# Performance work log

Measured on AMD Instinct MI355X. Metric: run time of the kernel, lower is better.

## Reference

```python
import jax, jax.numpy as jnp
import numpy as np

N_HEAD = 8

def _l2norm(x, eps=1e-12):
    # F.normalize(p=2, dim=-1): x / max(||x||_2, eps)
    return x / jnp.maximum(jnp.linalg.norm(x, axis=-1, keepdims=True), eps)

def setup_inputs() -> dict:
    key = jax.random.key(0)
    ks = jax.random.split(key, 9)
    B, L, E = 2, 2048, 512
    s = 0.02
    return {
        "query": jax.random.normal(ks[0], (B, L, E), dtype=jnp.float32),
        "Wq": s * jax.random.normal(ks[1], (E, E), dtype=jnp.float32),
        "bq": jnp.zeros((E,), dtype=jnp.float32),
        "Wk": s * jax.random.normal(ks[2], (E, E), dtype=jnp.float32),
        "bk": jnp.zeros((E,), dtype=jnp.float32),
        "Wv": s * jax.random.normal(ks[3], (E, E), dtype=jnp.float32),
        "bv": jnp.zeros((E,), dtype=jnp.float32),
        "Wo": s * jax.random.normal(ks[4], (E, E), dtype=jnp.float32),
        "bo": jnp.zeros((E,), dtype=jnp.float32),
    }

def reference(query, Wq, bq, Wk, bk, Wv, bv, Wo, bo):
    B, L, E = query.shape
    H = N_HEAD
    hd = E // H
    # Faithful to torch: .view(tgt_len, bsz, E) is a RESHAPE, not a transpose.
    x = query.reshape(L, B, E)
    q = jax.nn.relu(x @ Wq.T + bq)
    k = jax.nn.relu(x @ Wk.T + bk)
    v = x @ Wv.T + bv
    q = _l2norm(q)
    k = _l2norm(k)
    # (L, B, E) -> (L, B*H, hd) -> (B*H, L, hd)
    q_ = q.reshape(L, B * H, hd).transpose(1, 0, 2)
    k_ = k.reshape(L, B * H, hd).transpose(1, 0, 2)
    v_ = v.reshape(L, B * H, hd).transpose(1, 0, 2)
    # Causal linear attention: cumulative outer-product of k,v then contract with q.
    kv = jnp.einsum('nld,nlm->nldm', k_, v_)      # [B*H, L, hd, hd]
    kv_cum = jnp.cumsum(kv, axis=1)
    out = jnp.einsum('nld,nldm->nlm', q_, kv_cum)  # [B*H, L, hd]
    out = out.transpose(1, 0, 2).reshape(L, B, E)
    out = out @ Wo.T + bo
    return out.reshape(B, L, E)
```

## Files before the change

### kernel.cpp

```cpp
#include <hip/hip_runtime.h>
#include <hip/hip_bf16.h>

typedef __attribute__((ext_vector_type(8))) short short8;
typedef __attribute__((ext_vector_type(4))) float f32x4;
using bf16 = __hip_bfloat16;

__device__ __forceinline__ unsigned short f2bf(float f) {
    unsigned u = __float_as_uint(f);
    u += 0x7fff + ((u >> 16) & 1);
    return (unsigned short)(u >> 16);
}
__device__ __forceinline__ float bf2f(unsigned short s) {
    return __uint_as_float(((unsigned)s) << 16);
}
__device__ __forceinline__ void gl_lds16(const unsigned short* g, unsigned short* l) {
    __builtin_amdgcn_global_load_lds(
        (const __attribute__((address_space(1))) unsigned int*)g,
        (__attribute__((address_space(3))) unsigned int*)l, 16, 0, 0);
}


__global__ __launch_bounds__(256) void pack_kernel(
    const float* __restrict__ X, const float* __restrict__ Wq, const float* __restrict__ Wk,
    const float* __restrict__ Wv, const float* __restrict__ Wo,
    bf16* __restrict__ Xp, bf16* __restrict__ Wqp, bf16* __restrict__ Wkp,
    bf16* __restrict__ Wvp, bf16* __restrict__ Wop, float* __restrict__ ssq)
{
    __shared__ __align__(16) unsigned short sm[4096];
    int id = blockIdx.x;
    int tid = threadIdx.x;
    if (id < 8) {
        int zi = id * 1024 + tid * 4;
        *(float4*)&ssq[zi] = make_float4(0.f, 0.f, 0.f, 0.f);
    }
    const float* src; unsigned short* dst; int g, sc;
    if (id < 512) { src = X; dst = (unsigned short*)Xp; g = id >> 3; sc = id & 7; }
    else {
        int t = id - 512; int wsel = t >> 6; int u = t & 63;
        g = u >> 3; sc = u & 7;
        src = (wsel == 0) ? Wq : ((wsel == 1) ? Wk : ((wsel == 2) ? Wv : Wo));
        dst = (unsigned short*)((wsel == 0) ? Wqp : ((wsel == 1) ? Wkp : ((wsel == 2) ? Wvp : Wop)));
    }
    int r = tid >> 2, kq = tid & 3;
    const float* sp = src + (size_t)(g * 64 + r) * 512 + sc * 64 + kq * 16;
    #pragma unroll
    for (int i = 0; i < 4; ++i) {
        float4 v = *(const float4*)(sp + i * 4);
        int kk = kq * 16 + i * 4;
        int sl = kk >> 3, el = kk & 7;
        ushort4 u4;
        u4.x = f2bf(v.x); u4.y = f2bf(v.y); u4.z = f2bf(v.z); u4.w = f2bf(v.w);
        *(ushort4*)&sm[(sl * 64 + r) * 8 + el] = u4;
    }
    __syncthreads();
    unsigned short* dp = dst + (size_t)g * 32768 + sc * 4096;
    *(uint4*)(dp + tid * 16)     = *(const uint4*)&sm[tid * 16];
    *(uint4*)(dp + tid * 16 + 8) = *(const uint4*)&sm[tid * 16 + 8];
}

__global__ __launch_bounds__(256) void qkv_gemm_kernel(
    const bf16* __restrict__ Xp,
    const bf16* __restrict__ W0p, const bf16* __restrict__ W1p, const bf16* __restrict__ W2p,
    const float* __restrict__ b0, const float* __restrict__ b1, const float* __restrict__ b2,
    bf16* __restrict__ O0, bf16* __restrict__ O1, bf16* __restrict__ O2,
    float* __restrict__ ssq)
{
    __shared__ __align__(16) unsigned short smem[8192];
    unsigned short* As = smem;
    unsigned short* Bs = smem + 2048;
    int z = blockIdx.z;
    const unsigned short* Wg = (const unsigned short*)((z == 0) ? W0p : ((z == 1) ? W1p : W2p));
    const float* bias = (z == 0) ? b0 : ((z == 1) ? b1 : b2);
    unsigned short* Out = (unsigned short*)((z == 0) ? O0 : ((z == 1) ? O1 : O2));
    const unsigned short* Ag = (const unsigned short*)Xp;

    int g  = blockIdx.x;
    int gB = blockIdx.y * 2;
    int m0 = g * 64;
    int n0 = blockIdx.y * 128;
    int tid = threadIdx.x;
    int lane = tid & 63;
    int w = tid >> 6;
    int wm = (w >> 1) * 32;
    int wn = (w & 1) * 64;
    int fr = lane & 15, qf = lane >> 4;

    f32x4 zero4 = {0.f, 0.f, 0.f, 0.f};
    f32x4 acc[2][4];
    #pragma unroll
    for (int t = 0; t < 2; ++t)
        #pragma unroll
        for (int u = 0; u < 4; ++u) acc[t][u] = zero4;

    for (int kw = 0; kw < 16; ++kw) {
        int s0 = kw * 4;
        __syncthreads();
        gl_lds16(Ag + ((size_t)(g * 64 + s0 + w) * 64 + lane) * 8, As + w * 512);
        gl_lds16(Wg + ((size_t)(gB * 64 + s0 + w) * 64 + lane) * 8, Bs + w * 1024);
        gl_lds16(Wg + ((size_t)((gB + 1) * 64 + s0 + w) * 64 + lane) * 8, Bs + w * 1024 + 512);
        __syncthreads();
        short8 af[2], bfr[4];
        #pragma unroll
        for (int t = 0; t < 2; ++t) af[t] = *(const short8*)&As[(qf * 64 + wm + t * 16 + fr) * 8];
        #pragma unroll
        for (int u = 0; u < 4; ++u) bfr[u] = *(const short8*)&Bs[(qf * 128 + wn + u * 16 + fr) * 8];
        #pragma unroll
        for (int t = 0; t < 2; ++t)
            #pragma unroll
            for (int u = 0; u < 4; ++u)
                acc[t][u] = __builtin_amdgcn_mfma_f32_16x16x32_bf16(af[t], bfr[u], acc[t][u], 0, 0, 0);
    }

    bool relu = (z < 2);
    int rb = qf * 4;
    #pragma unroll
    for (int t = 0; t < 2; ++t)
        #pragma unroll
        for (int u = 0; u < 4; ++u) {
            float bv = bias[n0 + wn + u * 16 + fr];
            #pragma unroll
            for (int r = 0; r < 4; ++r) {
                float v = acc[t][u][r] + bv;
                if (relu) v = fmaxf(v, 0.f);
                acc[t][u][r] = v;
            }
        }
    if (relu) {
        #pragma unroll
        for (int t = 0; t < 2; ++t)
            #pragma unroll
            for (int r = 0; r < 4; ++r) {
                float s = 0.f;
                #pragma unroll
                for (int u = 0; u < 4; ++u) s += acc[t][u][r] * acc[t][u][r];
                #pragma unroll
                for (int off = 1; off < 16; off <<= 1) s += __shfl_xor(s, off, 64);
                if (fr == 0) atomicAdd(&ssq[z * 4096 + m0 + wm + t * 16 + rb + r], s);
            }
    }
    __syncthreads();
    #pragma unroll
    for (int t = 0; t < 2; ++t)
        #pragma unroll
        for (int u = 0; u < 4; ++u)
            #pragma unroll
            for (int r = 0; r < 4; ++r)
                smem[(wm + t * 16 + rb + r) * 128 + wn + u * 16 + fr] = f2bf(acc[t][u][r]);
    __syncthreads();
    #pragma unroll
    for (int rep = 0; rep < 4; ++rep) {
        int idx8 = rep * 256 + tid;
        int row = idx8 >> 4, col8 = (idx8 & 15) * 8;
        *(uint4*)(Out + (size_t)(m0 + row) * 512 + n0 + col8) = *(const uint4*)&smem[row * 128 + col8];
    }
}

__global__ __launch_bounds__(256) void chunk_kv_kernel(
    const bf16* __restrict__ Kb, const bf16* __restrict__ Vb,
    const float* __restrict__ ssq, float* __restrict__ ScT, bf16* __restrict__ Vt_g)
{
    int n = blockIdx.x >> 4, c = blockIdx.x & 15;
    int b = n >> 3, h = n & 7;
    __shared__ float Ks[64 * 64];
    __shared__ float Vs[64 * 64];
    const unsigned short* Kg = (const unsigned short*)Kb;
    const unsigned short* Vg = (const unsigned short*)Vb;
    int tid = threadIdx.x;
    int td = tid >> 4, tm = tid & 15;
    int d0 = td * 4, m0 = tm * 4;
    int vm = tid & 63, vj0 = (tid >> 6) * 16;
    float acc[4][4] = {};
    for (int half = 0; half < 2; ++half) {
        __syncthreads();
        #pragma unroll
        for (int rep = 0; rep < 4; ++rep) {
            int idx = rep * 1024 + tid * 4;
            int j = idx >> 6, d = idx & 63;
            int grow = (c * 128 + half * 64 + j) * 2 + b;
            ushort4 ku = *(const ushort4*)&Kg[(size_t)grow * 512 + h * 64 + d];
            ushort4 vu = *(const ushort4*)&Vg[(size_t)grow * 512 + h * 64 + d];
            float rk = 1.f / fmaxf(sqrtf(ssq[4096 + grow]), 1e-12f);
            *(float4*)&Ks[j * 64 + d] = make_float4(bf2f(ku.x), bf2f(ku.y), bf2f(ku.z), bf2f(ku.w));
            *(float4*)&Vs[j * 64 + d] = make_float4(bf2f(vu.x) * rk, bf2f(vu.y) * rk,
                                                    bf2f(vu.z) * rk, bf2f(vu.w) * rk);
        }
        __syncthreads();
        for (int j = 0; j < 64; ++j) {
            float4 kv = *(const float4*)&Ks[j * 64 + d0];
            float4 vv = *(const float4*)&Vs[j * 64 + m0];
            acc[0][0] += kv.x*vv.x; acc[0][1] += kv.x*vv.y; acc[0][2] += kv.x*vv.z; acc[0][3] += kv.x*vv.w;
            acc[1][0] += kv.y*vv.x; acc[1][1] += kv.y*vv.y; acc[1][2] += kv.y*vv.z; acc[1][3] += kv.y*vv.w;
            acc[2][0] += kv.z*vv.x; acc[2][1] += kv.z*vv.y; acc[2][2] += kv.z*vv.z; acc[2][3] += kv.z*vv.w;
            acc[3][0] += kv.w*vv.x; acc[3][1] += kv.w*vv.y; acc[3][2] += kv.w*vv.z; acc[3][3] += kv.w*vv.w;
        }
        unsigned short tmp[16];
        #pragma unroll
        for (int i = 0; i < 16; ++i) tmp[i] = f2bf(Vs[(vj0 + i) * 64 + vm]);
        size_t vtoff = (size_t)n * 131072 + (size_t)vm * 2048 + c * 128 + half * 64 + vj0;
        *(uint4*)((unsigned short*)Vt_g + vtoff)     = *(uint4*)&tmp[0];
        *(uint4*)((unsigned short*)Vt_g + vtoff + 8) = *(uint4*)&tmp[8];
    }
    float* outp = ScT + (size_t)blockIdx.x * 4096;
    #pragma unroll
    for (int j2 = 0; j2 < 4; ++j2) {
        float4 o4 = make_float4(acc[0][j2], acc[1][j2], acc[2][j2], acc[3][j2]);
        *(float4*)&outp[(m0 + j2) * 64 + d0] = o4;
    }
}

__global__ __launch_bounds__(256) void prefix_kernel(const float* __restrict__ ScT, bf16* __restrict__ SpT)
{
    int n = blockIdx.x >> 4;
    int idx = ((blockIdx.x & 15) << 8) + threadIdx.x;
    size_t base = (size_t)n * 65536 + idx;
    unsigned short* sp = (unsigned short*)SpT;
    float run = 0.f;
    #pragma unroll
    for (int c = 0; c < 16; ++c) {
        size_t off = base + (size_t)c * 4096;
        sp[off] = f2bf(run);
        run += ScT[off];
    }
}

__global__ __launch_bounds__(256) void attn_kernel(
    const bf16* __restrict__ Qb, const bf16* __restrict__ Kb,
    const bf16* __restrict__ Vt_g, const bf16* __restrict__ SpT_g,
    const float* __restrict__ ssq, bf16* __restrict__ AOb)
{
    int n = blockIdx.x >> 4, c = blockIdx.x & 15;
    int b = n >> 3, h = n & 7;
    __shared__ unsigned short Qs[128 * 72];
    __shared__ unsigned short Ks[128 * 72];
    __shared__ unsigned short Vt[64 * 136];
    __shared__ unsigned short Ps[4 * 32 * 40];
    int tid = threadIdx.x;
    int lane = tid & 63;
    int w = tid >> 6;
    int fr = lane & 15, q = lane >> 4;

    const unsigned short* Qg = (const unsigned short*)Qb;
    const unsigned short* Kg = (const unsigned short*)Kb;
    const unsigned short* Vg = (const unsigned short*)Vt_g;

    #pragma unroll
    for (int rep = 0; rep < 4; ++rep) {
        int idx = rep * 256 + tid;
        int l = idx >> 3, dc = (idx & 7) * 8;
        size_t goff = (size_t)((c * 128 + l) * 2 + b) * 512 + h * 64 + dc;
        *(uint4*)&Qs[l * 72 + dc] = *(const uint4*)(Qg + goff);
        *(uint4*)&Ks[l * 72 + dc] = *(const uint4*)(Kg + goff);
    }
    #pragma unroll
    for (int rep = 0; rep < 4; ++rep) {
        int idx = rep * 256 + tid;
        int m = idx >> 4, jc = (idx & 15) * 8;
        *(uint4*)&Vt[m * 136 + jc] =
            *(const uint4*)(Vg + (size_t)n * 131072 + (size_t)m * 2048 + c * 128 + jc);
    }
    __syncthreads();

    short8 qf[2][2];
    #pragma unroll
    for (int lt = 0; lt < 2; ++lt)
        #pragma unroll
        for (int kh = 0; kh < 2; ++kh)
            qf[lt][kh] = *(const short8*)&Qs[(w * 32 + lt * 16 + fr) * 72 + kh * 32 + q * 8];

    f32x4 zero4 = {0.f, 0.f, 0.f, 0.f};
    f32x4 oacc[2][4];
    #pragma unroll
    for (int lt = 0; lt < 2; ++lt)
        #pragma unroll
        for (int mt = 0; mt < 4; ++mt) oacc[lt][mt] = zero4;

    const unsigned short* spg = (const unsigned short*)SpT_g + (size_t)blockIdx.x * 4096;
    #pragma unroll
    for (int mt = 0; mt < 4; ++mt) {
        #pragma unroll
        for (int kh = 0; kh < 2; ++kh) {
            short8 sf = *(const short8*)&spg[(mt * 16 + fr) * 64 + kh * 32 + q * 8];
            oacc[0][mt] = __builtin_amdgcn_mfma_f32_16x16x32_bf16(qf[0][kh], sf, oacc[0][mt], 0, 0, 0);
            oacc[1][mt] = __builtin_amdgcn_mfma_f32_16x16x32_bf16(qf[1][kh], sf, oacc[1][mt], 0, 0, 0);
        }
    }

    unsigned short* myPs = &Ps[w * 1280];
    int rbase = q * 4;
    for (int jt = 0; jt <= w; ++jt) {
        f32x4 pacc[2][2];
        pacc[0][0] = zero4; pacc[0][1] = zero4; pacc[1][0] = zero4; pacc[1][1] = zero4;
        #pragma unroll
        for (int jt16 = 0; jt16 < 2; ++jt16) {
            #pragma unroll
            for (int kh = 0; kh < 2; ++kh) {
                short8 kf = *(const short8*)&Ks[(jt * 32 + jt16 * 16 + fr) * 72 + kh * 32 + q * 8];
                pacc[0][jt16] = __builtin_amdgcn_mfma_f32_16x16x32_bf16(qf[0][kh], kf, pacc[0][jt16], 0, 0, 0);
                pacc[1][jt16] = __builtin_amdgcn_mfma_f32_16x16x32_bf16(qf[1][kh], kf, pacc[1][jt16], 0, 0, 0);
            }
        }
        bool diag = (jt == w);
        #pragma unroll
        for (int lt = 0; lt < 2; ++lt)
            #pragma unroll
            for (int jt16 = 0; jt16 < 2; ++jt16)
                #pragma unroll
                for (int r = 0; r < 4; ++r) {
                    int ll = lt * 16 + rbase + r;
                    int jl = jt16 * 16 + fr;
                    float pv = pacc[lt][jt16][r];
                    if (diag && jl > ll) pv = 0.f;
                    myPs[ll * 40 + jl] = f2bf(pv);
                }
        short8 pf0 = *(const short8*)&myPs[fr * 40 + q * 8];
        short8 pf1 = *(const short8*)&myPs[(16 + fr) * 40 + q * 8];
        #pragma unroll
        for (int mt = 0; mt < 4; ++mt) {
            short8 vf = *(const short8*)&Vt[(mt * 16 + fr) * 136 + jt * 32 + q * 8];
            oacc[0][mt] = __builtin_amdgcn_mfma_f32_16x16x32_bf16(pf0, vf, oacc[0][mt], 0, 0, 0);
            oacc[1][mt] = __builtin_amdgcn_mfma_f32_16x16x32_bf16(pf1, vf, oacc[1][mt], 0, 0, 0);
        }
    }

    float rqv[2][4];
    #pragma unroll
    for (int lt = 0; lt < 2; ++lt)
        #pragma unroll
        for (int r = 0; r < 4; ++r) {
            int flat = (c * 128 + w * 32 + lt * 16 + rbase + r) * 2 + b;
            rqv[lt][r] = 1.f / fmaxf(sqrtf(ssq[flat]), 1e-12f);
        }
    __syncthreads();
    #pragma unroll
    for (int lt = 0; lt < 2; ++lt)
        #pragma unroll
        for (int mt = 0; mt < 4; ++mt)
            #pragma unroll
            for (int r = 0; r < 4; ++r)
                Qs[(w * 32 + lt * 16 + rbase + r) * 64 + mt * 16 + fr] = f2bf(oacc[lt][mt][r] * rqv[lt][r]);
    __syncthreads();
    #pragma unroll
    for (int rep = 0; rep < 4; ++rep) {
        int idx8 = rep * 256 + tid;
        int l = idx8 >> 3, m8 = (idx8 & 7) * 8;
        *(uint4*)((unsigned short*)AOb + (size_t)((c * 128 + l) * 2 + b) * 512 + h * 64 + m8) =
            *(const uint4*)&Qs[l * 64 + m8];
    }
}

__global__ __launch_bounds__(256) void oproj_kernel(
    const bf16* __restrict__ A, const bf16* __restrict__ Wop,
    const float* __restrict__ bias, float* __restrict__ Out)
{
    __shared__ __align__(16) unsigned short smem[16384];
    unsigned short* As = smem;
    unsigned short* Bs = smem + 2560;
    const unsigned short* Ag = (const unsigned short*)A;
    const unsigned short* Wg = (const unsigned short*)Wop;
    int m0 = blockIdx.x * 64;
    int gB = blockIdx.y * 2;
    int n0 = blockIdx.y * 128;
    int tid = threadIdx.x;
    int lane = tid & 63;
    int w = tid >> 6;
    int fr = lane & 15, qf = lane >> 4;
    int wm = (w >> 1) * 32;
    int wn = (w & 1) * 64;
    int srow = tid >> 2;
    int skk  = (tid & 3) * 8;

    f32x4 zero4 = {0.f, 0.f, 0.f, 0.f};
    f32x4 acc[2][4];
    #pragma unroll
    for (int t = 0; t < 2; ++t)
        #pragma unroll
        for (int u = 0; u < 4; ++u) acc[t][u] = zero4;

    for (int kw = 0; kw < 16; ++kw) {
        int k0 = kw * 32, s0 = kw * 4;
        __syncthreads();
        *(uint4*)&As[srow * 40 + skk] = *(const uint4*)(Ag + (size_t)(m0 + srow) * 512 + k0 + skk);
        gl_lds16(Wg + ((size_t)(gB * 64 + s0 + w) * 64 + lane) * 8, Bs + w * 1024);
        gl_lds16(Wg + ((size_t)((gB + 1) * 64 + s0 + w) * 64 + lane) * 8, Bs + w * 1024 + 512);
        __syncthreads();
        short8 af[2], bfr[4];
        #pragma unroll
        for (int t = 0; t < 2; ++t) af[t] = *(const short8*)&As[(wm + t * 16 + fr) * 40 + qf * 8];
        #pragma unroll
        for (int u = 0; u < 4; ++u) bfr[u] = *(const short8*)&Bs[(qf * 128 + wn + u * 16 + fr) * 8];
        #pragma unroll
        for (int t = 0; t < 2; ++t)
            #pragma unroll
            for (int u = 0; u < 4; ++u)
                acc[t][u] = __builtin_amdgcn_mfma_f32_16x16x32_bf16(af[t], bfr[u], acc[t][u], 0, 0, 0);
    }

    int rb = qf * 4;
    float* Cf = (float*)smem;
    __syncthreads();
    #pragma unroll
    for (int t = 0; t < 2; ++t)
        #pragma unroll
        for (int u = 0; u < 4; ++u) {
            float bv = bias[n0 + wn + u * 16 + fr];
            #pragma unroll
            for (int r = 0; r < 4; ++r)
                Cf[(wm + t * 16 + rb + r) * 128 + wn + u * 16 + fr] = acc[t][u][r] + bv;
        }
    __syncthreads();
    #pragma unroll
    for (int rep = 0; rep < 8; ++rep) {
        int idx = rep * 256 + tid;
        int row = idx >> 5, c4 = (idx & 31) * 4;
        *(float4*)(Out + (size_t)(m0 + row) * 512 + n0 + c4) = *(const float4*)&Cf[row * 128 + c4];
    }
}

extern "C" void kernel_launch(void* const* d_in, const int* in_sizes, int n_in,
                              void* d_out, int out_size, void* d_ws, size_t ws_size,
                              hipStream_t stream)
{
    (void)in_sizes; (void)n_in; (void)out_size; (void)ws_size;
    const float* x  = (const float*)d_in[0];
    const float* Wq = (const float*)d_in[1];
    const float* bq = (const float*)d_in[2];
    const float* Wk = (const float*)d_in[3];
    const float* bk = (const float*)d_in[4];
    const float* Wv = (const float*)d_in[5];
    const float* bv = (const float*)d_in[6];
    const float* Wo = (const float*)d_in[7];
    const float* bo = (const float*)d_in[8];
    float* out = (float*)d_out;

    float* ssq = (float*)d_ws;
    bf16* Xp  = (bf16*)(ssq + 8192);
    bf16* Wqp = Xp + 2097152;
    bf16* Wkp = Wqp + 262144;
    bf16* Wvp = Wkp + 262144;
    bf16* Wop = Wvp + 262144;
    bf16* Qb  = Wop + 262144;
    bf16* Kb  = Qb + 2097152;
    bf16* Vb  = Kb + 2097152;
    bf16* Vt  = Vb + 2097152;
    bf16* AOb = Vt + 2097152;
    bf16* SpT = AOb + 2097152;
    float* ScT = (float*)(SpT + 1048576);

    pack_kernel<<<768, 256, 0, stream>>>(x, Wq, Wk, Wv, Wo, Xp, Wqp, Wkp, Wvp, Wop, ssq);
    qkv_gemm_kernel<<<dim3(64, 4, 3), 256, 0, stream>>>(Xp, Wqp, Wkp, Wvp, bq, bk, bv, Qb, Kb, Vb, ssq);
    chunk_kv_kernel<<<dim3(256), 256, 0, stream>>>(Kb, Vb, ssq, ScT, Vt);
    prefix_kernel<<<dim3(256), 256, 0, stream>>>(ScT, SpT);
    attn_kernel<<<dim3(256), 256, 0, stream>>>(Qb, Kb, Vt, SpT, ssq, AOb);
    oproj_kernel<<<dim3(64, 4), 256, 0, stream>>>(AOb, Wop, bo, out);
}
```

Before: 123.6 us.

## Fuse all six stages into one cooperative persistent kernel with grid syncs

Replaces the six separate kernel launches (pack, QKV GEMM, chunk KV, prefix, attention, output projection) with one cooperative kernel of 256 blocks that runs each stage in turn, separated by grid-wide barriers. The aim is to remove per-launch overhead and the idle gaps between dependent kernels. In exchange each stage is limited to 256 blocks: the pack and QKV stages now loop over several work items per block, which lowers parallelism there. The single kernel also uses a larger shared-memory footprint, which may reduce occupancy.

After: 315.1 us. 155% more time.

```diff
diff --git a/kernel.cpp b/kernel.cpp
--- a/kernel.cpp
+++ b/kernel.cpp
@@ -1,5 +1,8 @@
 #include <hip/hip_runtime.h>
 #include <hip/hip_bf16.h>
+#include <hip/hip_cooperative_groups.h>
+
+namespace cg = cooperative_groups;
 
 typedef __attribute__((ext_vector_type(8))) short short8;
 typedef __attribute__((ext_vector_type(4))) float f32x4;
@@ -20,399 +23,385 @@
 }
 
 
-__global__ __launch_bounds__(256) void pack_kernel(
-    const float* __restrict__ X, const float* __restrict__ Wq, const float* __restrict__ Wk,
-    const float* __restrict__ Wv, const float* __restrict__ Wo,
+__global__ __launch_bounds__(256) void fused_kernel(
+    const float* __restrict__ X,
+    const float* __restrict__ Wq, const float* __restrict__ bq,
+    const float* __restrict__ Wk, const float* __restrict__ bk,
+    const float* __restrict__ Wv, const float* __restrict__ bv,
+    const float* __restrict__ Wo, const float* __restrict__ bo,
+    float* __restrict__ out,
     bf16* __restrict__ Xp, bf16* __restrict__ Wqp, bf16* __restrict__ Wkp,
-    bf16* __restrict__ Wvp, bf16* __restrict__ Wop, float* __restrict__ ssq)
+    bf16* __restrict__ Wvp, bf16* __restrict__ Wop,
+    bf16* __restrict__ Qb, bf16* __restrict__ Kb, bf16* __restrict__ Vb,
+    bf16* __restrict__ Vt_g, bf16* __restrict__ AOb, bf16* __restrict__ SpT,
+    float* __restrict__ ScT, float* __restrict__ ssq)
 {
-    __shared__ __align__(16) unsigned short sm[4096];
-    int id = blockIdx.x;
-    int tid = threadIdx.x;
-    if (id < 8) {
-        int zi = id * 1024 + tid * 4;
-        *(float4*)&ssq[zi] = make_float4(0.f, 0.f, 0.f, 0.f);
-    }
-    const float* src; unsigned short* dst; int g, sc;
-    if (id < 512) { src = X; dst = (unsigned short*)Xp; g = id >> 3; sc = id & 7; }
-    else {
-        int t = id - 512; int wsel = t >> 6; int u = t & 63;
-        g = u >> 3; sc = u & 7;
-        src = (wsel == 0) ? Wq : ((wsel == 1) ? Wk : ((wsel == 2) ? Wv : Wo));
-        dst = (unsigned short*)((wsel == 0) ? Wqp : ((wsel == 1) ? Wkp : ((wsel == 2) ? Wvp : Wop)));
-    }
-    int r = tid >> 2, kq = tid & 3;
-    const float* sp = src + (size_t)(g * 64 + r) * 512 + sc * 64 + kq * 16;
-    #pragma unroll
-    for (int i = 0; i < 4; ++i) {
-        float4 v = *(const float4*)(sp + i * 4);
-        int kk = kq * 16 + i * 4;
-        int sl = kk >> 3, el = kk & 7;
-        ushort4 u4;
-        u4.x = f2bf(v.x); u4.y = f2bf(v.y); u4.z = f2bf(v.z); u4.w = f2bf(v.w);
-        *(ushort4*)&sm[(sl * 64 + r) * 8 + el] = u4;
-    }
-    __syncthreads();
-    unsigned short* dp = dst + (size_t)g * 32768 + sc * 4096;
-    *(uint4*)(dp + tid * 16)     = *(const uint4*)&sm[tid * 16];
-    *(uint4*)(dp + tid * 16 + 8) = *(const uint4*)&sm[tid * 16 + 8];
-}
-
-__global__ __launch_bounds__(256) void qkv_gemm_kernel(
-    const bf16* __restrict__ Xp,
-    const bf16* __restrict__ W0p, const bf16* __restrict__ W1p, const bf16* __restrict__ W2p,
-    const float* __restrict__ b0, const float* __restrict__ b1, const float* __restrict__ b2,
-    bf16* __restrict__ O0, bf16* __restrict__ O1, bf16* __restrict__ O2,
-    float* __restrict__ ssq)
-{
-    __shared__ __align__(16) unsigned short smem[8192];
-    unsigned short* As = smem;
-    unsigned short* Bs = smem + 2048;
-    int z = blockIdx.z;
-    const unsigned short* Wg = (const unsigned short*)((z == 0) ? W0p : ((z == 1) ? W1p : W2p));
-    const float* bias = (z == 0) ? b0 : ((z == 1) ? b1 : b2);
-    unsigned short* Out = (unsigned short*)((z == 0) ? O0 : ((z == 1) ? O1 : O2));
-    const unsigned short* Ag = (const unsigned short*)Xp;
-
-    int g  = blockIdx.x;
-    int gB = blockIdx.y * 2;
-    int m0 = g * 64;
-    int n0 = blockIdx.y * 128;
-    int tid = threadIdx.x;
-    int lane = tid & 63;
-    int w = tid >> 6;
-    int wm = (w >> 1) * 32;
-    int wn = (w & 1) * 64;
-    int fr = lane & 15, qf = lane >> 4;
-
-    f32x4 zero4 = {0.f, 0.f, 0.f, 0.f};
-    f32x4 acc[2][4];
-    #pragma unroll
-    for (int t = 0; t < 2; ++t)
-        #pragma unroll
-        for (int u = 0; u < 4; ++u) acc[t][u] = zero4;
-
-    for (int kw = 0; kw < 16; ++kw) {
-        int s0 = kw * 4;
-        __syncthreads();
-        gl_lds16(Ag + ((size_t)(g * 64 + s0 + w) * 64 + lane) * 8, As + w * 512);
-        gl_lds16(Wg + ((size_t)(gB * 64 + s0 + w) * 64 + lane) * 8, Bs + w * 1024);
-        gl_lds16(Wg + ((size_t)((gB + 1) * 64 + s0 + w) * 64 + lane) * 8, Bs + w * 1024 + 512);
-        __syncthreads();
-        short8 af[2], bfr[4];
-        #pragma unroll
-        for (int t = 0; t < 2; ++t) af[t] = *(const short8*)&As[(qf * 64 + wm + t * 16 + fr) * 8];
-        #pragma unroll
-        for (int u = 0; u < 4; ++u) bfr[u] = *(const short8*)&Bs[(qf * 128 + wn + u * 16 + fr) * 8];
-        #pragma unroll
-        for (int t = 0; t < 2; ++t)
-            #pragma unroll
-            for (int u = 0; u < 4; ++u)
-                acc[t][u] = __builtin_amdgcn_mfma_f32_16x16x32_bf16(af[t], bfr[u], acc[t][u], 0, 0, 0);
-    }
-
-    bool relu = (z < 2);
-    int rb = qf * 4;
-    #pragma unroll
-    for (int t = 0; t < 2; ++t)
-        #pragma unroll
-        for (int u = 0; u < 4; ++u) {
-            float bv = bias[n0 + wn + u * 16 + fr];
-            #pragma unroll
-            for (int r = 0; r < 4; ++r) {
-                float v = acc[t][u][r] + bv;
-                if (relu) v = fmaxf(v, 0.f);
-                acc[t][u][r] = v;
-            }
-        }
-    if (relu) {
-        #pragma unroll
-        for (int t = 0; t < 2; ++t)
-            #pragma unroll
-            for (int r = 0; r < 4; ++r) {
-                float s = 0.f;
-                #pragma unroll
-                for (int u = 0; u < 4; ++u) s += acc[t][u][r] * acc[t][u][r];
-                #pragma unroll
-                for (int off = 1; off < 16; off <<= 1) s += __shfl_xor(s, off, 64);
-                if (fr == 0) atomicAdd(&ssq[z * 4096 + m0 + wm + t * 16 + rb + r], s);
-            }
-    }
-    __syncthreads();
-    #pragma unroll
-    for (int t = 0; t < 2; ++t)
-        #pragma unroll
-        for (int u = 0; u < 4; ++u)
-            #pragma unroll
-            for (int r = 0; r < 4; ++r)
-                smem[(wm + t * 16 + rb + r) * 128 + wn + u * 16 + fr] = f2bf(acc[t][u][r]);
-    __syncthreads();
-    #pragma unroll
-    for (int rep = 0; rep < 4; ++rep) {
-        int idx8 = rep * 256 + tid;
-        int row = idx8 >> 4, col8 = (idx8 & 15) * 8;
-        *(uint4*)(Out + (size_t)(m0 + row) * 512 + n0 + col8) = *(const uint4*)&smem[row * 128 + col8];
-    }
-}
-
-__global__ __launch_bounds__(256) void chunk_kv_kernel(
-    const bf16* __restrict__ Kb, const bf16* __restrict__ Vb,
-    const float* __restrict__ ssq, float* __restrict__ ScT, bf16* __restrict__ Vt_g)
-{
-    int n = blockIdx.x >> 4, c = blockIdx.x & 15;
-    int b = n >> 3, h = n & 7;
-    __shared__ float Ks[64 * 64];
-    __shared__ float Vs[64 * 64];
-    const unsigned short* Kg = (const unsigned short*)Kb;
-    const unsigned short* Vg = (const unsigned short*)Vb;
-    int tid = threadIdx.x;
-    int td = tid >> 4, tm = tid & 15;
-    int d0 = td * 4, m0 = tm * 4;
-    int vm = tid & 63, vj0 = (tid >> 6) * 16;
-    float acc[4][4] = {};
-    for (int half = 0; half < 2; ++half) {
-        __syncthreads();
-        #pragma unroll
-        for (int rep = 0; rep < 4; ++rep) {
-            int idx = rep * 1024 + tid * 4;
-            int j = idx >> 6, d = idx & 63;
-            int grow = (c * 128 + half * 64 + j) * 2 + b;
-            ushort4 ku = *(const ushort4*)&Kg[(size_t)grow * 512 + h * 64 + d];
-            ushort4 vu = *(const ushort4*)&Vg[(size_t)grow * 512 + h * 64 + d];
-            float rk = 1.f / fmaxf(sqrtf(ssq[4096 + grow]), 1e-12f);
-            *(float4*)&Ks[j * 64 + d] = make_float4(bf2f(ku.x), bf2f(ku.y), bf2f(ku.z), bf2f(ku.w));
-            *(float4*)&Vs[j * 64 + d] = make_float4(bf2f(vu.x) * rk, bf2f(vu.y) * rk,
-                                                    bf2f(vu.z) * rk, bf2f(vu.w) * rk);
-        }
-        __syncthreads();
-        for (int j = 0; j < 64; ++j) {
-            float4 kv = *(const float4*)&Ks[j * 64 + d0];
-            float4 vv = *(const float4*)&Vs[j * 64 + m0];
-            acc[0][0] += kv.x*vv.x; acc[0][1] += kv.x*vv.y; acc[0][2] += kv.x*vv.z; acc[0][3] += kv.x*vv.w;
-            acc[1][0] += kv.y*vv.x; acc[1][1] += kv.y*vv.y; acc[1][2] += kv.y*vv.z; acc[1][3] += kv.y*vv.w;
-            acc[2][0] += kv.z*vv.x; acc[2][1] += kv.z*vv.y; acc[2][2] += kv.z*vv.z; acc[2][3] += kv.z*vv.w;
-            acc[3][0] += kv.w*vv.x; acc[3][1] += kv.w*vv.y; acc[3][2] += kv.w*vv.z; acc[3][3] += kv.w*vv.w;
-        }
-        unsigned short tmp[16];
-        #pragma unroll
-        for (int i = 0; i < 16; ++i) tmp[i] = f2bf(Vs[(vj0 + i) * 64 + vm]);
-        size_t vtoff = (size_t)n * 131072 + (size_t)vm * 2048 + c * 128 + half * 64 + vj0;
-        *(uint4*)((unsigned short*)Vt_g + vtoff)     = *(uint4*)&tmp[0];
-        *(uint4*)((unsigned short*)Vt_g + vtoff + 8) = *(uint4*)&tmp[8];
-    }
-    float* outp = ScT + (size_t)blockIdx.x * 4096;
-    #pragma unroll
-    for (int j2 = 0; j2 < 4; ++j2) {
-        float4 o4 = make_float4(acc[0][j2], acc[1][j2], acc[2][j2], acc[3][j2]);
-        *(float4*)&outp[(m0 + j2) * 64 + d0] = o4;
-    }
-}
-
-__global__ __launch_bounds__(256) void prefix_kernel(const float* __restrict__ ScT, bf16* __restrict__ SpT)
-{
-    int n = blockIdx.x >> 4;
-    int idx = ((blockIdx.x & 15) << 8) + threadIdx.x;
-    size_t base = (size_t)n * 65536 + idx;
-    unsigned short* sp = (unsigned short*)SpT;
-    float run = 0.f;
-    #pragma unroll
-    for (int c = 0; c < 16; ++c) {
-        size_t off = base + (size_t)c * 4096;
-        sp[off] = f2bf(run);
-        run += ScT[off];
-    }
-}
-
-__global__ __launch_bounds__(256) void attn_kernel(
-    const bf16* __restrict__ Qb, const bf16* __restrict__ Kb,
-    const bf16* __restrict__ Vt_g, const bf16* __restrict__ SpT_g,
-    const float* __restrict__ ssq, bf16* __restrict__ AOb)
-{
-    int n = blockIdx.x >> 4, c = blockIdx.x & 15;
-    int b = n >> 3, h = n & 7;
-    __shared__ unsigned short Qs[128 * 72];
-    __shared__ unsigned short Ks[128 * 72];
-    __shared__ unsigned short Vt[64 * 136];
-    __shared__ unsigned short Ps[4 * 32 * 40];
+    __shared__ __align__(16) unsigned short SM[32256];
+    cg::grid_group grid = cg::this_grid();
+    int blk = blockIdx.x;
     int tid = threadIdx.x;
     int lane = tid & 63;
     int w = tid >> 6;
     int fr = lane & 15, q = lane >> 4;
-
-    const unsigned short* Qg = (const unsigned short*)Qb;
-    const unsigned short* Kg = (const unsigned short*)Kb;
-    const unsigned short* Vg = (const unsigned short*)Vt_g;
-
-    #pragma unroll
-    for (int rep = 0; rep < 4; ++rep) {
-        int idx = rep * 256 + tid;
-        int l = idx >> 3, dc = (idx & 7) * 8;
-        size_t goff = (size_t)((c * 128 + l) * 2 + b) * 512 + h * 64 + dc;
-        *(uint4*)&Qs[l * 72 + dc] = *(const uint4*)(Qg + goff);
-        *(uint4*)&Ks[l * 72 + dc] = *(const uint4*)(Kg + goff);
-    }
-    #pragma unroll
-    for (int rep = 0; rep < 4; ++rep) {
-        int idx = rep * 256 + tid;
-        int m = idx >> 4, jc = (idx & 15) * 8;
-        *(uint4*)&Vt[m * 136 + jc] =
-            *(const uint4*)(Vg + (size_t)n * 131072 + (size_t)m * 2048 + c * 128 + jc);
-    }
-    __syncthreads();
-
-    short8 qf[2][2];
-    #pragma unroll
-    for (int lt = 0; lt < 2; ++lt)
-        #pragma unroll
-        for (int kh = 0; kh < 2; ++kh)
-            qf[lt][kh] = *(const short8*)&Qs[(w * 32 + lt * 16 + fr) * 72 + kh * 32 + q * 8];
-
     f32x4 zero4 = {0.f, 0.f, 0.f, 0.f};
-    f32x4 oacc[2][4];
-    #pragma unroll
-    for (int lt = 0; lt < 2; ++lt)
-        #pragma unroll
-        for (int mt = 0; mt < 4; ++mt) oacc[lt][mt] = zero4;
-
-    const unsigned short* spg = (const unsigned short*)SpT_g + (size_t)blockIdx.x * 4096;
-    #pragma unroll
-    for (int mt = 0; mt < 4; ++mt) {
-        #pragma unroll
-        for (int kh = 0; kh < 2; ++kh) {
-            short8 sf = *(const short8*)&spg[(mt * 16 + fr) * 64 + kh * 32 + q * 8];
-            oacc[0][mt] = __builtin_amdgcn_mfma_f32_16x16x32_bf16(qf[0][kh], sf, oacc[0][mt], 0, 0, 0);
-            oacc[1][mt] = __builtin_amdgcn_mfma_f32_16x16x32_bf16(qf[1][kh], sf, oacc[1][mt], 0, 0, 0);
-        }
-    }
-
-    unsigned short* myPs = &Ps[w * 1280];
-    int rbase = q * 4;
-    for (int jt = 0; jt <= w; ++jt) {
-        f32x4 pacc[2][2];
-        pacc[0][0] = zero4; pacc[0][1] = zero4; pacc[1][0] = zero4; pacc[1][1] = zero4;
-        #pragma unroll
-        for (int jt16 = 0; jt16 < 2; ++jt16) {
+
+    {
+        unsigned short* sm = SM;
+        #pragma unroll
+        for (int rr = 0; rr < 3; ++rr) {
+            int id = blk * 3 + rr;
+            __syncthreads();
+            if (id < 8) {
+                int zi = id * 1024 + tid * 4;
+                *(float4*)&ssq[zi] = make_float4(0.f, 0.f, 0.f, 0.f);
+            }
+            const float* src; unsigned short* dst; int g, sc;
+            if (id < 512) { src = X; dst = (unsigned short*)Xp; g = id >> 3; sc = id & 7; }
+            else {
+                int t = id - 512; int wsel = t >> 6; int u = t & 63;
+                g = u >> 3; sc = u & 7;
+                src = (wsel == 0) ? Wq : ((wsel == 1) ? Wk : ((wsel == 2) ? Wv : Wo));
+                dst = (unsigned short*)((wsel == 0) ? Wqp : ((wsel == 1) ? Wkp : ((wsel == 2) ? Wvp : Wop)));
+            }
+            int r = tid >> 2, kq = tid & 3;
+            const float* sp = src + (size_t)(g * 64 + r) * 512 + sc * 64 + kq * 16;
+            #pragma unroll
+            for (int i = 0; i < 4; ++i) {
+                float4 v = *(const float4*)(sp + i * 4);
+                int kk = kq * 16 + i * 4;
+                int sl = kk >> 3, el = kk & 7;
+                ushort4 u4;
+                u4.x = f2bf(v.x); u4.y = f2bf(v.y); u4.z = f2bf(v.z); u4.w = f2bf(v.w);
+                *(ushort4*)&sm[(sl * 64 + r) * 8 + el] = u4;
+            }
+            __syncthreads();
+            unsigned short* dp = dst + (size_t)g * 32768 + sc * 4096;
+            *(uint4*)(dp + tid * 16)     = *(const uint4*)&sm[tid * 16];
+            *(uint4*)(dp + tid * 16 + 8) = *(const uint4*)&sm[tid * 16 + 8];
+        }
+    }
+    grid.sync();
+
+    {
+        unsigned short* As = SM;
+        unsigned short* Bs = SM + 2048;
+        const unsigned short* Ag = (const unsigned short*)Xp;
+        int g = blk & 63, gy = blk >> 6, gB = gy * 2;
+        int m0 = g * 64, n0 = gy * 128;
+        int wm = (w >> 1) * 32;
+        int wn = (w & 1) * 64;
+        for (int z = 0; z < 3; ++z) {
+            const unsigned short* Wg = (const unsigned short*)((z == 0) ? Wqp : ((z == 1) ? Wkp : Wvp));
+            const float* bias = (z == 0) ? bq : ((z == 1) ? bk : bv);
+            unsigned short* Out = (unsigned short*)((z == 0) ? Qb : ((z == 1) ? Kb : Vb));
+            f32x4 acc[2][4];
+            #pragma unroll
+            for (int t = 0; t < 2; ++t)
+                #pragma unroll
+                for (int u = 0; u < 4; ++u) acc[t][u] = zero4;
+
+            for (int kw = 0; kw < 16; ++kw) {
+                int s0 = kw * 4;
+                __syncthreads();
+                gl_lds16(Ag + ((size_t)(g * 64 + s0 + w) * 64 + lane) * 8, As + w * 512);
+                gl_lds16(Wg + ((size_t)(gB * 64 + s0 + w) * 64 + lane) * 8, Bs + w * 1024);
+                gl_lds16(Wg + ((size_t)((gB + 1) * 64 + s0 + w) * 64 + lane) * 8, Bs + w * 1024 + 512);
+                __syncthreads();
+                short8 af[2], bfr[4];
+                #pragma unroll
+                for (int t = 0; t < 2; ++t) af[t] = *(const short8*)&As[(q * 64 + wm + t * 16 + fr) * 8];
+                #pragma unroll
+                for (int u = 0; u < 4; ++u) bfr[u] = *(const short8*)&Bs[(q * 128 + wn + u * 16 + fr) * 8];
+                #pragma unroll
+                for (int t = 0; t < 2; ++t)
+                    #pragma unroll
+                    for (int u = 0; u < 4; ++u)
+                        acc[t][u] = __builtin_amdgcn_mfma_f32_16x16x32_bf16(af[t], bfr[u], acc[t][u], 0, 0, 0);
+            }
+
+            bool relu = (z < 2);
+            int rb = q * 4;
+            #pragma unroll
+            for (int t = 0; t < 2; ++t)
+                #pragma unroll
+                for (int u = 0; u < 4; ++u) {
+                    float bv2 = bias[n0 + wn + u * 16 + fr];
+                    #pragma unroll
+                    for (int r = 0; r < 4; ++r) {
+                        float v = acc[t][u][r] + bv2;
+                        if (relu) v = fmaxf(v, 0.f);
+                        acc[t][u][r] = v;
+                    }
+                }
+            if (relu) {
+                #pragma unroll
+                for (int t = 0; t < 2; ++t)
+                    #pragma unroll
+                    for (int r = 0; r < 4; ++r) {
+                        float s = 0.f;
+                        #pragma unroll
+                        for (int u = 0; u < 4; ++u) s += acc[t][u][r] * acc[t][u][r];
+                        #pragma unroll
+                        for (int off = 1; off < 16; off <<= 1) s += __shfl_xor(s, off, 64);
+                        if (fr == 0) atomicAdd(&ssq[z * 4096 + m0 + wm + t * 16 + rb + r], s);
+                    }
+            }
+            __syncthreads();
+            #pragma unroll
+            for (int t = 0; t < 2; ++t)
+                #pragma unroll
+                for (int u = 0; u < 4; ++u)
+                    #pragma unroll
+                    for (int r = 0; r < 4; ++r)
+                        SM[(wm + t * 16 + rb + r) * 128 + wn + u * 16 + fr] = f2bf(acc[t][u][r]);
+            __syncthreads();
+            #pragma unroll
+            for (int rep = 0; rep < 4; ++rep) {
+                int idx8 = rep * 256 + tid;
+                int row = idx8 >> 4, col8 = (idx8 & 15) * 8;
+                *(uint4*)(Out + (size_t)(m0 + row) * 512 + n0 + col8) = *(const uint4*)&SM[row * 128 + col8];
+            }
+        }
+    }
+    grid.sync();
+
+    {
+        float* Ksf = (float*)SM;
+        float* Vsf = Ksf + 4096;
+        const unsigned short* Kg = (const unsigned short*)Kb;
+        const unsigned short* Vg = (const unsigned short*)Vb;
+        int n = blk >> 4, c = blk & 15;
+        int b = n >> 3, h = n & 7;
+        int td = tid >> 4, tm = tid & 15;
+        int d0 = td * 4, m0 = tm * 4;
+        int vm = tid & 63, vj0 = (tid >> 6) * 16;
+        float acc[4][4] = {};
+        for (int half = 0; half < 2; ++half) {
+            __syncthreads();
+            #pragma unroll
+            for (int rep = 0; rep < 4; ++rep) {
+                int idx = rep * 1024 + tid * 4;
+                int j = idx >> 6, d = idx & 63;
+                int grow = (c * 128 + half * 64 + j) * 2 + b;
+                ushort4 ku = *(const ushort4*)&Kg[(size_t)grow * 512 + h * 64 + d];
+                ushort4 vu = *(const ushort4*)&Vg[(size_t)grow * 512 + h * 64 + d];
+                float rk = 1.f / fmaxf(sqrtf(ssq[4096 + grow]), 1e-12f);
+                *(float4*)&Ksf[j * 64 + d] = make_float4(bf2f(ku.x), bf2f(ku.y), bf2f(ku.z), bf2f(ku.w));
+                *(float4*)&Vsf[j * 64 + d] = make_float4(bf2f(vu.x) * rk, bf2f(vu.y) * rk,
+                                                         bf2f(vu.z) * rk, bf2f(vu.w) * rk);
+            }
+            __syncthreads();
+            for (int j = 0; j < 64; ++j) {
+                float4 kv = *(const float4*)&Ksf[j * 64 + d0];
+                float4 vv = *(const float4*)&Vsf[j * 64 + m0];
+                acc[0][0] += kv.x*vv.x; acc[0][1] += kv.x*vv.y; acc[0][2] += kv.x*vv.z; acc[0][3] += kv.x*vv.w;
+                acc[1][0] += kv.y*vv.x; acc[1][1] += kv.y*vv.y; acc[1][2] += kv.y*vv.z; acc[1][3] += kv.y*vv.w;
+                acc[2][0] += kv.z*vv.x; acc[2][1] += kv.z*vv.y; acc[2][2] += kv.z*vv.z; acc[2][3] += kv.z*vv.w;
+                acc[3][0] += kv.w*vv.x; acc[3][1] += kv.w*vv.y; acc[3][2] += kv.w*vv.z; acc[3][3] += kv.w*vv.w;
+            }
+            unsigned short tmp[16];
+            #pragma unroll
+            for (int i = 0; i < 16; ++i) tmp[i] = f2bf(Vsf[(vj0 + i) * 64 + vm]);
+            size_t vtoff = (size_t)n * 131072 + (size_t)vm * 2048 + c * 128 + half * 64 + vj0;
+            *(uint4*)((unsigned short*)Vt_g + vtoff)     = *(uint4*)&tmp[0];
+            *(uint4*)((unsigned short*)Vt_g + vtoff + 8) = *(uint4*)&tmp[8];
+        }
+        float* outp = ScT + (size_t)blk * 4096;
+        #pragma unroll
+        for (int j2 = 0; j2 < 4; ++j2) {
+            float4 o4 = make_float4(acc[0][j2], acc[1][j2], acc[2][j2], acc[3][j2]);
+            *(float4*)&outp[(m0 + j2) * 64 + d0] = o4;
+        }
+    }
+    grid.sync();
+
+    {
+        int n = blk >> 4;
+        int idx = ((blk & 15) << 8) + tid;
+        size_t base = (size_t)n * 65536 + idx;
+        unsigned short* sp = (unsigned short*)SpT;
+        float run = 0.f;
+        #pragma unroll
+        for (int c = 0; c < 16; ++c) {
+            size_t off = base + (size_t)c * 4096;
+            sp[off] = f2bf(run);
+            run += ScT[off];
+        }
+    }
+    grid.sync();
+
+    {
+        unsigned short* Qs  = SM;
+        unsigned short* Ks2 = SM + 9216;
+        unsigned short* Vts = SM + 18432;
+        unsigned short* Ps  = SM + 27136;
+        int n = blk >> 4, c = blk & 15;
+        int b = n >> 3, h = n & 7;
+        const unsigned short* Qg = (const unsigned short*)Qb;
+        const unsigned short* Kg = (const unsigned short*)Kb;
+        const unsigned short* Vg = (const unsigned short*)Vt_g;
+
+        #pragma unroll
+        for (int rep = 0; rep < 4; ++rep) {
+            int idx = rep * 256 + tid;
+            int l = idx >> 3, dc = (idx & 7) * 8;
+            size_t goff = (size_t)((c * 128 + l) * 2 + b) * 512 + h * 64 + dc;
+            *(uint4*)&Qs[l * 72 + dc]  = *(const uint4*)(Qg + goff);
+            *(uint4*)&Ks2[l * 72 + dc] = *(const uint4*)(Kg + goff);
+        }
+        #pragma unroll
+        for (int rep = 0; rep < 4; ++rep) {
+            int idx = rep * 256 + tid;
+            int m = idx >> 4, jc = (idx & 15) * 8;
+            *(uint4*)&Vts[m * 136 + jc] =
+                *(const uint4*)(Vg + (size_t)n * 131072 + (size_t)m * 2048 + c * 128 + jc);
+        }
+        __syncthreads();
+
+        short8 qfr[2][2];
+        #pragma unroll
+        for (int lt = 0; lt < 2; ++lt)
+            #pragma unroll
+            for (int kh = 0; kh < 2; ++kh)
+                qfr[lt][kh] = *(const short8*)&Qs[(w * 32 + lt * 16 + fr) * 72 + kh * 32 + q * 8];
+
+        f32x4 oacc[2][4];
+        #pragma unroll
+        for (int lt = 0; lt < 2; ++lt)
+            #pragma unroll
+            for (int mt = 0; mt < 4; ++mt) oacc[lt][mt] = zero4;
+
+        const unsigned short* spg = (const unsigned short*)SpT + (size_t)blk * 4096;
+        #pragma unroll
+        for (int mt = 0; mt < 4; ++mt) {
             #pragma unroll
             for (int kh = 0; kh < 2; ++kh) {
-                short8 kf = *(const short8*)&Ks[(jt * 32 + jt16 * 16 + fr) * 72 + kh * 32 + q * 8];
-                pacc[0][jt16] = __builtin_amdgcn_mfma_f32_16x16x32_bf16(qf[0][kh], kf, pacc[0][jt16], 0, 0, 0);
-                pacc[1][jt16] = __builtin_amdgcn_mfma_f32_16x16x32_bf16(qf[1][kh], kf, pacc[1][jt16], 0, 0, 0);
-            }
-        }
-        bool diag = (jt == w);
+                short8 sf = *(const short8*)&spg[(mt * 16 + fr) * 64 + kh * 32 + q * 8];
+                oacc[0][mt] = __builtin_amdgcn_mfma_f32_16x16x32_bf16(qfr[0][kh], sf, oacc[0][mt], 0, 0, 0);
+                oacc[1][mt] = __builtin_amdgcn_mfma_f32_16x16x32_bf16(qfr[1][kh], sf, oacc[1][mt], 0, 0, 0);
+            }
+        }
+
+        unsigned short* myPs = &Ps[w * 1280];
+        int rbase = q * 4;
+        for (int jt = 0; jt <= w; ++jt) {
+            f32x4 pacc[2][2];
+            pacc[0][0] = zero4; pacc[0][1] = zero4; pacc[1][0] = zero4; pacc[1][1] = zero4;
+            #pragma unroll
+            for (int jt16 = 0; jt16 < 2; ++jt16) {
+                #pragma unroll
+                for (int kh = 0; kh < 2; ++kh) {
+                    short8 kf = *(const short8*)&Ks2[(jt * 32 + jt16 * 16 + fr) * 72 + kh * 32 + q * 8];
+                    pacc[0][jt16] = __builtin_amdgcn_mfma_f32_16x16x32_bf16(qfr[0][kh], kf, pacc[0][jt16], 0, 0, 0);
+                    pacc[1][jt16] = __builtin_amdgcn_mfma_f32_16x16x32_bf16(qfr[1][kh], kf, pacc[1][jt16], 0, 0, 0);
+                }
+            }
+            bool diag = (jt == w);
+            #pragma unroll
+            for (int lt = 0; lt < 2; ++lt)
+                #pragma unroll
+                for (int jt16 = 0; jt16 < 2; ++jt16)
+                    #pragma unroll
+                    for (int r = 0; r < 4; ++r) {
+                        int ll = lt * 16 + rbase + r;
+                        int jl = jt16 * 16 + fr;
+                        float pv = pacc[lt][jt16][r];
+                        if (diag && jl > ll) pv = 0.f;
+                        myPs[ll * 40 + jl] = f2bf(pv);
+                    }
+            short8 pf0 = *(const short8*)&myPs[fr * 40 + q * 8];
+            short8 pf1 = *(const short8*)&myPs[(16 + fr) * 40 + q * 8];
+            #pragma unroll
+            for (int mt = 0; mt < 4; ++mt) {
+                short8 vf = *(const short8*)&Vts[(mt * 16 + fr) * 136 + jt * 32 + q * 8];
+                oacc[0][mt] = __builtin_amdgcn_mfma_f32_16x16x32_bf16(pf0, vf, oacc[0][mt], 0, 0, 0);
+                oacc[1][mt] = __builtin_amdgcn_mfma_f32_16x16x32_bf16(pf1, vf, oacc[1][mt], 0, 0, 0);
+            }
+        }
+
+        float rqv[2][4];
         #pragma unroll
         for (int lt = 0; lt < 2; ++lt)
             #pragma unroll
-            for (int jt16 = 0; jt16 < 2; ++jt16)
-                #pragma unroll
-                for (int r = 0; r < 4; ++r) {
-                    int ll = lt * 16 + rbase + r;
-                    int jl = jt16 * 16 + fr;
-                    float pv = pacc[lt][jt16][r];
-                    if (diag && jl > ll) pv = 0.f;
-                    myPs[ll * 40 + jl] = f2bf(pv);
-                }
-        short8 pf0 = *(const short8*)&myPs[fr * 40 + q * 8];
-        short8 pf1 = *(const short8*)&myPs[(16 + fr) * 40 + q * 8];
-        #pragma unroll
-        for (int mt = 0; mt < 4; ++mt) {
-            short8 vf = *(const short8*)&Vt[(mt * 16 + fr) * 136 + jt * 32 + q * 8];
-            oacc[0][mt] = __builtin_amdgcn_mfma_f32_16x16x32_bf16(pf0, vf, oacc[0][mt], 0, 0, 0);
-            oacc[1][mt] = __builtin_amdgcn_mfma_f32_16x16x32_bf16(pf1, vf, oacc[1][mt], 0, 0, 0);
-        }
-    }
-
-    float rqv[2][4];
-    #pragma unroll
-    for (int lt = 0; lt < 2; ++lt)
-        #pragma unroll
-        for (int r = 0; r < 4; ++r) {
-            int flat = (c * 128 + w * 32 + lt * 16 + rbase + r) * 2 + b;
-            rqv[lt][r] = 1.f / fmaxf(sqrtf(ssq[flat]), 1e-12f);
-        }
-    __syncthreads();
-    #pragma unroll
-    for (int lt = 0; lt < 2; ++lt)
-        #pragma unroll
-        for (int mt = 0; mt < 4; ++mt)
-            #pragma unroll
-            for (int r = 0; r < 4; ++r)
-                Qs[(w * 32 + lt * 16 + rbase + r) * 64 + mt * 16 + fr] = f2bf(oacc[lt][mt][r] * rqv[lt][r]);
-    __syncthreads();
-    #pragma unroll
-    for (int rep = 0; rep < 4; ++rep) {
-        int idx8 = rep * 256 + tid;
-        int l = idx8 >> 3, m8 = (idx8 & 7) * 8;
-        *(uint4*)((unsigned short*)AOb + (size_t)((c * 128 + l) * 2 + b) * 512 + h * 64 + m8) =
-            *(const uint4*)&Qs[l * 64 + m8];
-    }
-}
-
-__global__ __launch_bounds__(256) void oproj_kernel(
-    const bf16* __restrict__ A, const bf16* __restrict__ Wop,
-    const float* __restrict__ bias, float* __restrict__ Out)
-{
-    __shared__ __align__(16) unsigned short smem[16384];
-    unsigned short* As = smem;
-    unsigned short* Bs = smem + 2560;
-    const unsigned short* Ag = (const unsigned short*)A;
-    const unsigned short* Wg = (const unsigned short*)Wop;
-    int m0 = blockIdx.x * 64;
-    int gB = blockIdx.y * 2;
-    int n0 = blockIdx.y * 128;
-    int tid = threadIdx.x;
-    int lane = tid & 63;
-    int w = tid >> 6;
-    int fr = lane & 15, qf = lane >> 4;
-    int wm = (w >> 1) * 32;
-    int wn = (w & 1) * 64;
-    int srow = tid >> 2;
-    int skk  = (tid & 3) * 8;
-
-    f32x4 zero4 = {0.f, 0.f, 0.f, 0.f};
-    f32x4 acc[2][4];
-    #pragma unroll
-    for (int t = 0; t < 2; ++t)
-        #pragma unroll
-        for (int u = 0; u < 4; ++u) acc[t][u] = zero4;
-
-    for (int kw = 0; kw < 16; ++kw) {
-        int k0 = kw * 32, s0 = kw * 4;
+            for (int r = 0; r < 4; ++r) {
+                int flat = (c * 128 + w * 32 + lt * 16 + rbase + r) * 2 + b;
+                rqv[lt][r] = 1.f / fmaxf(sqrtf(ssq[flat]), 1e-12f);
+            }
         __syncthreads();
-        *(uint4*)&As[srow * 40 + skk] = *(const uint4*)(Ag + (size_t)(m0 + srow) * 512 + k0 + skk);
-        gl_lds16(Wg + ((size_t)(gB * 64 + s0 + w) * 64 + lane) * 8, Bs + w * 1024);
-        gl_lds16(Wg + ((size_t)((gB + 1) * 64 + s0 + w) * 64 + lane) * 8, Bs + w * 1024 + 512);
+        #pragma unroll
+        for (int lt = 0; lt < 2; ++lt)
+            #pragma unroll
+            for (int mt = 0; mt < 4; ++mt)
+                #pragma unroll
+                for (int r = 0; r < 4; ++r)
+                    Qs[(w * 32 + lt * 16 + rbase + r) * 64 + mt * 16 + fr] = f2bf(oacc[lt][mt][r] * rqv[lt][r]);
         __syncthreads();
-        short8 af[2], bfr[4];
-        #pragma unroll
-        for (int t = 0; t < 2; ++t) af[t] = *(const short8*)&As[(wm + t * 16 + fr) * 40 + qf * 8];
-        #pragma unroll
-        for (int u = 0; u < 4; ++u) bfr[u] = *(const short8*)&Bs[(qf * 128 + wn + u * 16 + fr) * 8];
+        #pragma unroll
+        for (int rep = 0; rep < 4; ++rep) {
+            int idx8 = rep * 256 + tid;
+            int l = idx8 >> 3, m8 = (idx8 & 7) * 8;
+            *(uint4*)((unsigned short*)AOb + (size_t)((c * 128 + l) * 2 + b) * 512 + h * 64 + m8) =
+                *(const uint4*)&Qs[l * 64 + m8];
+        }
+    }
+    grid.sync();
+
+    {
+        unsigned short* As = SM;
+        unsigned short* Bs = SM + 2560;
+        const unsigned short* Ag = (const unsigned short*)AOb;
+        const unsigned short* Wg = (const unsigned short*)Wop;
+        int g = blk & 63, gy = blk >> 6, gB = gy * 2;
+        int m0 = g * 64, n0 = gy * 128;
+        int wm = (w >> 1) * 32;
+        int wn = (w & 1) * 64;
+        int srow = tid >> 2;
+        int skk  = (tid & 3) * 8;
+
+        f32x4 acc[2][4];
         #pragma unroll
         for (int t = 0; t < 2; ++t)
             #pragma unroll
-            for (int u = 0; u < 4; ++u)
-                acc[t][u] = __builtin_amdgcn_mfma_f32_16x16x32_bf16(af[t], bfr[u], acc[t][u], 0, 0, 0);
-    }
-
-    int rb = qf * 4;
-    float* Cf = (float*)smem;
-    __syncthreads();
-    #pragma unroll
-    for (int t = 0; t < 2; ++t)
-        #pragma unroll
-        for (int u = 0; u < 4; ++u) {
-            float bv = bias[n0 + wn + u * 16 + fr];
-            #pragma unroll
-            for (int r = 0; r < 4; ++r)
-                Cf[(wm + t * 16 + rb + r) * 128 + wn + u * 16 + fr] = acc[t][u][r] + bv;
-        }
-    __syncthreads();
-    #pragma unroll
-    for (int rep = 0; rep < 8; ++rep) {
-        int idx = rep * 256 + tid;
-        int row = idx >> 5, c4 = (idx & 31) * 4;
-        *(float4*)(Out + (size_t)(m0 + row) * 512 + n0 + c4) = *(const float4*)&Cf[row * 128 + c4];
+            for (int u = 0; u < 4; ++u) acc[t][u] = zero4;
+
+        for (int kw = 0; kw < 16; ++kw) {
+            int k0 = kw * 32, s0 = kw * 4;
+            __syncthreads();
+            *(uint4*)&As[srow * 40 + skk] = *(const uint4*)(Ag + (size_t)(m0 + srow) * 512 + k0 + skk);
+            gl_lds16(Wg + ((size_t)(gB * 64 + s0 + w) * 64 + lane) * 8, Bs + w * 1024);
+            gl_lds16(Wg + ((size_t)((gB + 1) * 64 + s0 + w) * 64 + lane) * 8, Bs + w * 1024 + 512);
+            __syncthreads();
+            short8 af[2], bfr[4];
+            #pragma unroll
+            for (int t = 0; t < 2; ++t) af[t] = *(const short8*)&As[(wm + t * 16 + fr) * 40 + q * 8];
+            #pragma unroll
+            for (int u = 0; u < 4; ++u) bfr[u] = *(const short8*)&Bs[(q * 128 + wn + u * 16 + fr) * 8];
+            #pragma unroll
+            for (int t = 0; t < 2; ++t)
+                #pragma unroll
+                for (int u = 0; u < 4; ++u)
+                    acc[t][u] = __builtin_amdgcn_mfma_f32_16x16x32_bf16(af[t], bfr[u], acc[t][u], 0, 0, 0);
+        }
+
+        int rb = q * 4;
+        float* Cf = (float*)SM;
+        __syncthreads();
+        #pragma unroll
+        for (int t = 0; t < 2; ++t)
+            #pragma unroll
+            for (int u = 0; u < 4; ++u) {
+                float bv2 = bo[n0 + wn + u * 16 + fr];
+                #pragma unroll
+                for (int r = 0; r < 4; ++r)
+                    Cf[(wm + t * 16 + rb + r) * 128 + wn + u * 16 + fr] = acc[t][u][r] + bv2;
+            }
+        __syncthreads();
+        #pragma unroll
+        for (int rep = 0; rep < 8; ++rep) {
+            int idx = rep * 256 + tid;
+            int row = idx >> 5, c4 = (idx & 31) * 4;
+            *(float4*)(out + (size_t)(m0 + row) * 512 + n0 + c4) = *(const float4*)&Cf[row * 128 + c4];
+        }
     }
 }
 
@@ -446,10 +435,12 @@
     bf16* SpT = AOb + 2097152;
     float* ScT = (float*)(SpT + 1048576);
 
-    pack_kernel<<<768, 256, 0, stream>>>(x, Wq, Wk, Wv, Wo, Xp, Wqp, Wkp, Wvp, Wop, ssq);
-    qkv_gemm_kernel<<<dim3(64, 4, 3), 256, 0, stream>>>(Xp, Wqp, Wkp, Wvp, bq, bk, bv, Qb, Kb, Vb, ssq);
-    chunk_kv_kernel<<<dim3(256), 256, 0, stream>>>(Kb, Vb, ssq, ScT, Vt);
-    prefix_kernel<<<dim3(256), 256, 0, stream>>>(ScT, SpT);
-    attn_kernel<<<dim3(256), 256, 0, stream>>>(Qb, Kb, Vt, SpT, ssq, AOb);
-    oproj_kernel<<<dim3(64, 4), 256, 0, stream>>>(AOb, Wop, bo, out);
+    void* args[] = {
+        (void*)&x, (void*)&Wq, (void*)&bq, (void*)&Wk, (void*)&bk,
+        (void*)&Wv, (void*)&bv, (void*)&Wo, (void*)&bo, (void*)&out,
+        (void*)&Xp, (void*)&Wqp, (void*)&Wkp, (void*)&Wvp, (void*)&Wop,
+        (void*)&Qb, (void*)&Kb, (void*)&Vb, (void*)&Vt, (void*)&AOb, (void*)&SpT,
+        (void*)&ScT, (void*)&ssq
+    };
+    hipLaunchCooperativeKernel((const void*)fused_kernel, dim3(256), dim3(256), args, 0, stream);
 }
```
